# Performance work log

Hardware: AMD Instinct MI355X
Metric: run time of the kernel (lower is better)

Reference implementation:

```python
import jax, jax.numpy as jnp
import numpy as np

D_OUT = 32


def mlp(x, Ws, bs):
    # Ws: (L+1, d, d), bs: (L+1, d); relu after hidden layers, linear output
    h = x
    n = Ws.shape[0]
    for i in range(n - 1):
        h = jax.nn.relu(h @ Ws[i] + bs[i])
    return h @ Ws[n - 1] + bs[n - 1]


def causal_dot_product(Q, K, V, t1, t2):
    """out[:,:,i] = Q_i @ sum_{j: t2[j] <= t1[i]} K_j V_j^T.
    t2 is sorted (timestamps), so the cumulative outer-product state can be
    computed with a cumsum and gathered via searchsorted.
    Q: (1,1,T1,d); K,V: (1,1,T2,d); t1: (T1,); t2: (T2,).
    """
    outer = K[..., :, :, None] * V[..., :, None, :]      # (1,1,T2,d,d)
    S = jnp.cumsum(outer, axis=2)                        # prefix states
    idx = jnp.searchsorted(t2, t1, side='right') - 1     # (T1,)
    valid = idx >= 0
    Sg = S[:, :, jnp.maximum(idx, 0)]                    # (1,1,T1,d,d)
    out = jnp.einsum('bhid,bhide->bhie', Q, Sg)
    return jnp.where(valid[None, None, :, None], out, jnp.zeros((), out.dtype))


def _with_sorted_time(x, key):
    T = x.shape[2]
    t = jnp.sort(jax.random.uniform(key, (T,), dtype=jnp.float32)) * 100.0
    return x.at[0, 0, :, -1].set(t)


def setup_inputs() -> dict:
    key = jax.random.key(0)
    ks = jax.random.split(key, 16)
    d = 64
    Ts = [4096, 6144, 8192, 4096]
    mods = {}
    for i, T in enumerate(Ts):
        x = jax.random.normal(ks[i], (1, 1, T, d), dtype=jnp.float32)
        mods[f'm{i+1}'] = _with_sorted_time(x, ks[8 + i])
    scale = 1.0 / np.sqrt(d)
    WQ_w = jax.random.normal(ks[4], (3, d, d), dtype=jnp.float32) * scale
    WQ_b = jnp.zeros((3, d), dtype=jnp.float32)
    WK_w = jax.random.normal(ks[5], (4, 3, d, d), dtype=jnp.float32) * scale
    WK_b = jnp.zeros((4, 3, d), dtype=jnp.float32)
    return dict(m1=mods['m1'], m2=mods['m2'], m3=mods['m3'], m4=mods['m4'],
                WQ_w=WQ_w, WQ_b=WQ_b, WK_w=WK_w, WK_b=WK_b)


def reference(m1, m2, m3, m4, WQ_w, WQ_b, WK_w, WK_b):
    Q = mlp(m1, WQ_w, WQ_b)            # (1,1,T1,d)
    t1 = m1[0, 0, :, -1]               # (T1,)
    total = None
    for mi, X in enumerate([m1, m2, m3, m4]):
        K = mlp(X, WK_w[mi], WK_b[mi])
        V = X
        t2 = X[0, 0, :, -1]
        Z = causal_dot_product(Q, K, V, t1, t2)  # (1,1,T1,d)
        total = Z if total is None else total + Z
    # cat over dim=1 then sum(1) == sum of per-modality results, dim 1 dropped
    yhat = total.sum(axis=1)[..., :D_OUT]        # (1,T1,d_out)
    return yhat
```

## Files before the change

### kernel.cpp

```cpp
#include <hip/hip_runtime.h>


#define QB_OFF   0
#define KB_OFF   131072
#define SP_OFF   851968
#define TD_OFF   1581056
#define C_OFF    1603584

typedef __attribute__((ext_vector_type(8))) short short8;
typedef __attribute__((ext_vector_type(4))) float floatx4;

__device__ __forceinline__ unsigned short f2bf(float f) {
    union { float f; unsigned u; } v; v.f = f;
    unsigned r = v.u + 0x7fff + ((v.u >> 16) & 1);
    return (unsigned short)(r >> 16);
}

#define MFMA16(a,b,c) __builtin_amdgcn_mfma_f32_16x16x32_bf16((a),(b),(c),0,0,0)

__global__ __launch_bounds__(256) void k_fused(
    const float* __restrict__ x0, const float* __restrict__ x1,
    const float* __restrict__ x2, const float* __restrict__ x3,
    const float* __restrict__ wq_w, const float* __restrict__ wq_b,
    const float* __restrict__ wk_w, const float* __restrict__ wk_b,
    float* __restrict__ ws)
{
    __shared__ unsigned short H0[128*72];
    __shared__ unsigned short H1[128*72];
    __shared__ unsigned short Wt[64*72];
    __shared__ unsigned short KT[64*136];
    __shared__ unsigned short VT[32*136];

    const int tid = threadIdx.x;
    const int bid = blockIdx.x;

    int task, rb;
    if (bid < 32)       { task = 0; rb = bid; }
    else if (bid < 64)  { task = 1; rb = bid - 32; }
    else if (bid < 112) { task = 2; rb = bid - 64; }
    else if (bid < 176) { task = 3; rb = bid - 112; }
    else                { task = 4; rb = bid - 176; }

    const float* Xs[4] = {x0, x1, x2, x3};
    const int rowoff[4] = {0, 4096, 10240, 18432};
    const int spoff[4]  = {0, 65, 162, 291};

    const float* X; const float* W; const float* Bv;
    int mm = -1;
    if (task == 0) { X = x0; W = wq_w; Bv = wq_b; }
    else {
        mm = task - 1;
        X = Xs[mm]; W = wk_w + mm*3*64*64; Bv = wk_b + mm*3*64;
    }

    const int row0 = rb * 128;

    {
        const float4* X4 = (const float4*)(X + (size_t)row0*64);
        #pragma unroll
        for (int k = 0; k < 8; ++k) {
            int idx = k*256 + tid;
            float4 v = X4[idx];
            int rr = idx >> 4, c4 = (idx & 15) * 4;
            ushort4 h;
            h.x = f2bf(v.x); h.y = f2bf(v.y); h.z = f2bf(v.z); h.w = f2bf(v.w);
            *(ushort4*)&H0[rr*72 + c4] = h;
        }
    }
    if (task > 0 && tid < 128)
        ws[TD_OFF + rowoff[mm] + row0 + tid] = X[(size_t)(row0 + tid)*64 + 63];

    const int w    = tid >> 6;
    const int lane = tid & 63;
    const int lm   = lane & 15;
    const int q    = lane >> 4;

    #pragma unroll 1
    for (int l = 0; l < 3; ++l) {
        __syncthreads();
        {
            const float4* W4 = (const float4*)(W + l*4096);
            #pragma unroll
            for (int k = 0; k < 4; ++k) {
                int idx = k*256 + tid;
                float4 v = W4[idx];
                int d = idx >> 4, c4 = (idx & 15) * 4;
                Wt[(c4+0)*72 + d] = f2bf(v.x);
                Wt[(c4+1)*72 + d] = f2bf(v.y);
                Wt[(c4+2)*72 + d] = f2bf(v.z);
                Wt[(c4+3)*72 + d] = f2bf(v.w);
            }
        }
        __syncthreads();

        const unsigned short* Hin  = (l & 1) ? H1 : H0;
        unsigned short*       Hout = (l & 1) ? H0 : H1;
        float bias = Bv[l*64 + w*16 + lm];
        short8 b0 = *(const short8*)&Wt[(w*16+lm)*72 + q*8];
        short8 b1 = *(const short8*)&Wt[(w*16+lm)*72 + 32 + q*8];
        #pragma unroll
        for (int mt = 0; mt < 8; ++mt) {
            floatx4 acc = {bias, bias, bias, bias};
            short8 a0 = *(const short8*)&Hin[(mt*16+lm)*72 + q*8];
            short8 a1 = *(const short8*)&Hin[(mt*16+lm)*72 + 32 + q*8];
            acc = MFMA16(a0, b0, acc);
            acc = MFMA16(a1, b1, acc);
            int r0 = mt*16 + q*4;
            #pragma unroll
            for (int r = 0; r < 4; ++r) {
                float f = acc[r];
                if (l < 2) f = fmaxf(f, 0.0f);
                unsigned short hb = f2bf(f);
                Hout[(r0+r)*72 + w*16 + lm] = hb;
                if (l == 2 && task > 0)
                    KT[(w*16+lm)*136 + r0 + r] = hb;
            }
        }
    }
    __syncthreads();

    {
        unsigned short* dst = (task == 0)
            ? (unsigned short*)(ws + QB_OFF)
            : (unsigned short*)(ws + KB_OFF) + (size_t)rowoff[mm]*64;
        #pragma unroll
        for (int k = 0; k < 8; ++k) {
            int idx = k*256 + tid;
            int rr = idx >> 4, c4 = (idx & 15) * 4;
            *(ushort4*)&dst[(size_t)(row0 + rr)*64 + c4] = *(ushort4*)&H1[rr*72 + c4];
        }
    }
    if (task == 0) return;

    {
        #pragma unroll
        for (int k = 0; k < 4; ++k) {
            int idx = k*256 + tid;
            int j = idx >> 3, e4 = (idx & 7) * 4;
            float4 v = *(const float4*)&X[(size_t)(row0 + j)*64 + e4];
            VT[(e4+0)*136 + j] = f2bf(v.x);
            VT[(e4+1)*136 + j] = f2bf(v.y);
            VT[(e4+2)*136 + j] = f2bf(v.z);
            VT[(e4+3)*136 + j] = f2bf(v.w);
        }
    }
    float* spbase = ws + SP_OFF + (size_t)spoff[mm]*2048;
    if (rb == 0)
        for (int idx = tid; idx < 2048; idx += 256) spbase[idx] = 0.0f;
    __syncthreads();

    #pragma unroll 1
    for (int c = 0; c < 2; ++c) {
        float* slot = spbase + (size_t)(2*rb + c + 1) * 2048;
        #pragma unroll
        for (int nt = 0; nt < 2; ++nt) {
            floatx4 acc = {0.f, 0.f, 0.f, 0.f};
            #pragma unroll
            for (int ks = 0; ks < 2; ++ks) {
                short8 a = *(const short8*)&KT[(w*16+lm)*136 + c*64 + ks*32 + q*8];
                short8 b = *(const short8*)&VT[(nt*16+lm)*136 + c*64 + ks*32 + q*8];
                acc = MFMA16(a, b, acc);
            }
            #pragma unroll
            for (int r = 0; r < 4; ++r) {
                int d = w*16 + q*4 + r;
                int e = nt*16 + lm;
                slot[d*32 + e] = acc[r];
            }
        }
    }
}

__global__ __launch_bounds__(64) void k_prefix(float* __restrict__ ws)
{
    const int nslots[4] = {65, 97, 129, 65};
    const int spoff[4]  = {0, 65, 162, 291};
    const int Tm[4]     = {4096, 6144, 8192, 4096};
    const int rowoff[4] = {0, 4096, 10240, 18432};
    const int bid = blockIdx.x;

    if (bid < 128) {
        const int m = bid >> 5;
        const int entry = (bid & 31)*64 + threadIdx.x;
        float* p = ws + SP_OFF + (size_t)spoff[m]*2048 + entry;
        const int n = nslots[m];
        float s = 0.0f;
        #pragma unroll 8
        for (int k = 0; k < n; ++k) {
            float v = p[(size_t)k*2048];
            s += v;
            p[(size_t)k*2048] = s;
        }
        return;
    }
    const float* td = ws + TD_OFF;
    int* ctab = (int*)(ws + C_OFF);
    #pragma unroll 1
    for (int k = 0; k < 4; ++k) {
        int g = (bid - 128)*256 + k*64 + threadIdx.x;
        int m = g >> 7;
        int tile = (g >> 1) & 63;
        int bound = g & 1;
        float t = td[tile*64 + (bound ? 63 : 0)];
        const float* t2 = td + rowoff[m];
        int lo = 0, hi = Tm[m];
        while (lo < hi) {
            int mid = (lo + hi) >> 1;
            if (t2[mid] <= t) lo = mid + 1; else hi = mid;
        }
        ctab[g] = lo;
    }
}

__global__ __launch_bounds__(256) void k_query(
    const float* __restrict__ x0, const float* __restrict__ x1,
    const float* __restrict__ x2, const float* __restrict__ x3,
    float* __restrict__ ws, float* __restrict__ out)
{
    __shared__ unsigned short qs[64*72];
    __shared__ unsigned short kc[64*72];
    __shared__ unsigned short vt[32*72];
    __shared__ unsigned short st[32*72];
    __shared__ unsigned short ps[64*72];
    __shared__ float tq[64];
    __shared__ float tcs[64];

    const int tid  = threadIdx.x;
    const int m    = blockIdx.x & 3;
    const int tile = blockIdx.x >> 2;
    const int i0   = tile * 64;

    const float* Xs[4] = {x0, x1, x2, x3};
    const int rowoff[4] = {0, 4096, 10240, 18432};
    const int spoff[4]  = {0, 65, 162, 291};
    const float* X = Xs[m];

    const int* ctab = (const int*)(ws + C_OFF);
    const int c_lo = ctab[m*128 + tile*2 + 0];
    const int c_hi = ctab[m*128 + tile*2 + 1];
    const int B0   = c_lo >> 6;
    const int Bhi  = (c_hi + 63) >> 6;

    const unsigned short* Qg = (const unsigned short*)(ws + QB_OFF);
    const unsigned short* Kg = (const unsigned short*)(ws + KB_OFF) + (size_t)rowoff[m]*64;
    const float* td = ws + TD_OFF;
    const float* sp = ws + SP_OFF + (size_t)(spoff[m] + B0)*2048;

    {
        #pragma unroll
        for (int k = 0; k < 4; ++k) {
            int idx = k*256 + tid;
            int rr = idx >> 4, c4 = (idx & 15) * 4;
            *(ushort4*)&qs[rr*72 + c4] = *(const ushort4*)&Qg[(size_t)(i0 + rr)*64 + c4];
        }
        #pragma unroll
        for (int k = 0; k < 8; ++k) {
            int idx = k*256 + tid;
            int d = idx >> 5, e = idx & 31;
            st[e*72 + d] = f2bf(sp[idx]);
        }
        if (tid < 64) tq[tid] = td[i0 + tid];
    }
    __syncthreads();

    const int w    = tid >> 6;
    const int lane = tid & 63;
    const int lm   = lane & 15;
    const int q    = lane >> 4;

    float t1v[16];
    #pragma unroll
    for (int mt = 0; mt < 4; ++mt)
        #pragma unroll
        for (int r = 0; r < 4; ++r)
            t1v[mt*4 + r] = tq[mt*16 + q*4 + r];

    short8 qa[4][2];
    #pragma unroll
    for (int mt = 0; mt < 4; ++mt) {
        qa[mt][0] = *(const short8*)&qs[(mt*16+lm)*72 + q*8];
        qa[mt][1] = *(const short8*)&qs[(mt*16+lm)*72 + 32 + q*8];
    }

    floatx4 accO[2];
    #pragma unroll
    for (int nt = 0; nt < 2; ++nt) {
        floatx4 acc = {0.f, 0.f, 0.f, 0.f};
        #pragma unroll
        for (int ks = 0; ks < 2; ++ks) {
            short8 b = *(const short8*)&st[(nt*16+lm)*72 + ks*32 + q*8];
            acc = MFMA16(qa[w][ks], b, acc);
        }
        accO[nt] = acc;
    }

    #pragma unroll 1
    for (int B = B0; B < Bhi; ++B) {
        __syncthreads();
        #pragma unroll
        for (int k = 0; k < 4; ++k) {
            int idx = k*256 + tid;
            int j = idx >> 4, c4 = (idx & 15) * 4;
            *(ushort4*)&kc[j*72 + c4] = *(const ushort4*)&Kg[(size_t)(B*64 + j)*64 + c4];
        }
        #pragma unroll
        for (int k = 0; k < 2; ++k) {
            int idx = k*256 + tid;
            int j = idx >> 3, e4 = (idx & 7) * 4;
            float4 v = *(const float4*)&X[(size_t)(B*64 + j)*64 + e4];
            vt[(e4+0)*72 + j] = f2bf(v.x);
            vt[(e4+1)*72 + j] = f2bf(v.y);
            vt[(e4+2)*72 + j] = f2bf(v.z);
            vt[(e4+3)*72 + j] = f2bf(v.w);
        }
        if (tid < 64) tcs[tid] = td[rowoff[m] + B*64 + tid];
        __syncthreads();

        {
            short8 bk0 = *(const short8*)&kc[(w*16+lm)*72 + q*8];
            short8 bk1 = *(const short8*)&kc[(w*16+lm)*72 + 32 + q*8];
            float t2j = tcs[w*16 + lm];
            #pragma unroll
            for (int mt = 0; mt < 4; ++mt) {
                floatx4 f = {0.f, 0.f, 0.f, 0.f};
                f = MFMA16(qa[mt][0], bk0, f);
                f = MFMA16(qa[mt][1], bk1, f);
                #pragma unroll
                for (int r = 0; r < 4; ++r) {
                    float p = (t2j <= t1v[mt*4 + r]) ? f[r] : 0.0f;
                    ps[(mt*16 + q*4 + r)*72 + w*16 + lm] = f2bf(p);
                }
            }
        }
        __syncthreads();

        {
            short8 pa0 = *(const short8*)&ps[(w*16+lm)*72 + q*8];
            short8 pa1 = *(const short8*)&ps[(w*16+lm)*72 + 32 + q*8];
            #pragma unroll
            for (int nt = 0; nt < 2; ++nt) {
                short8 bv0 = *(const short8*)&vt[(nt*16+lm)*72 + q*8];
                short8 bv1 = *(const short8*)&vt[(nt*16+lm)*72 + 32 + q*8];
                accO[nt] = MFMA16(pa0, bv0, accO[nt]);
                accO[nt] = MFMA16(pa1, bv1, accO[nt]);
            }
        }
    }

    #pragma unroll
    for (int nt = 0; nt < 2; ++nt)
        #pragma unroll
        for (int r = 0; r < 4; ++r) {
            int i = w*16 + q*4 + r;
            int e = nt*16 + lm;
            atomicAdd(&out[(size_t)(i0 + i)*32 + e], accO[nt][r]);
        }
}

extern "C" void kernel_launch(void* const* d_in, const int* in_sizes, int n_in,
                              void* d_out, int out_size, void* d_ws, size_t ws_size,
                              hipStream_t stream) {
    const float* x0   = (const float*)d_in[0];
    const float* x1   = (const float*)d_in[1];
    const float* x2   = (const float*)d_in[2];
    const float* x3   = (const float*)d_in[3];
    const float* wq_w = (const float*)d_in[4];
    const float* wq_b = (const float*)d_in[5];
    const float* wk_w = (const float*)d_in[6];
    const float* wk_b = (const float*)d_in[7];
    float* ws  = (float*)d_ws;
    float* out = (float*)d_out;

    hipMemsetAsync(out, 0, (size_t)out_size * sizeof(float), stream);
    hipLaunchKernelGGL(k_fused,  dim3(208), dim3(256), 0, stream,
                       x0, x1, x2, x3, wq_w, wq_b, wk_w, wk_b, ws);
    hipLaunchKernelGGL(k_prefix, dim3(130), dim3(64),  0, stream, ws);
    hipLaunchKernelGGL(k_query,  dim3(256), dim3(256), 0, stream,
                       x0, x1, x2, x3, ws, out);
}
```

Before: 115.6 us.

## Fuse MLP, prefix and query kernels into one cooperative kernel with grid syncs

Replaces the memset plus three separate kernel launches with a single cooperative kernel that uses grid-wide syncs between the MLP/state phase, the prefix-sum/searchsorted phase, and the query phase. Spare blocks zero the output in place of the memset. MLP weights are now held in registers, loaded directly from global memory, rather than staged through a transposed shared-memory tile, and shared memory is unioned across phases. The goal is to remove launch and inter-kernel gaps. In exchange, the prefix phase runs on only 32 blocks with longer per-thread chains, and the kernel pays for cooperative launch and grid barriers.

```diff
diff --git a/kernel.cpp b/kernel.cpp
--- a/kernel.cpp
+++ b/kernel.cpp
@@ -1,4 +1,7 @@
 #include <hip/hip_runtime.h>
+#include <hip/hip_cooperative_groups.h>
+
+namespace cg = cooperative_groups;
 
 
 #define QB_OFF   0
@@ -18,170 +21,177 @@
 
 #define MFMA16(a,b,c) __builtin_amdgcn_mfma_f32_16x16x32_bf16((a),(b),(c),0,0,0)
 
-__global__ __launch_bounds__(256) void k_fused(
+struct P1 {
+    unsigned short H[128*72];
+    unsigned short KT[64*136];
+    unsigned short VT[32*136];
+};
+struct P3 {
+    unsigned short qs[64*72];
+    unsigned short kc[64*72];
+    unsigned short vt[32*72];
+    unsigned short st[32*72];
+    unsigned short ps[64*72];
+    float tq[64];
+    float tcs[64];
+};
+union __align__(16) SMem { P1 p1; P3 p3; };
+
+__global__ __launch_bounds__(256) void k_all(
     const float* __restrict__ x0, const float* __restrict__ x1,
     const float* __restrict__ x2, const float* __restrict__ x3,
     const float* __restrict__ wq_w, const float* __restrict__ wq_b,
     const float* __restrict__ wk_w, const float* __restrict__ wk_b,
-    float* __restrict__ ws)
+    float* __restrict__ ws, float* __restrict__ out)
 {
-    __shared__ unsigned short H0[128*72];
-    __shared__ unsigned short H1[128*72];
-    __shared__ unsigned short Wt[64*72];
-    __shared__ unsigned short KT[64*136];
-    __shared__ unsigned short VT[32*136];
+    __shared__ SMem sm;
+    cg::grid_group grid = cg::this_grid();
 
     const int tid = threadIdx.x;
     const int bid = blockIdx.x;
-
-    int task, rb;
-    if (bid < 32)       { task = 0; rb = bid; }
-    else if (bid < 64)  { task = 1; rb = bid - 32; }
-    else if (bid < 112) { task = 2; rb = bid - 64; }
-    else if (bid < 176) { task = 3; rb = bid - 112; }
-    else                { task = 4; rb = bid - 176; }
-
     const float* Xs[4] = {x0, x1, x2, x3};
     const int rowoff[4] = {0, 4096, 10240, 18432};
     const int spoff[4]  = {0, 65, 162, 291};
-
-    const float* X; const float* W; const float* Bv;
-    int mm = -1;
-    if (task == 0) { X = x0; W = wq_w; Bv = wq_b; }
-    else {
-        mm = task - 1;
-        X = Xs[mm]; W = wk_w + mm*3*64*64; Bv = wk_b + mm*3*64;
-    }
-
-    const int row0 = rb * 128;
-
-    {
-        const float4* X4 = (const float4*)(X + (size_t)row0*64);
-        #pragma unroll
-        for (int k = 0; k < 8; ++k) {
-            int idx = k*256 + tid;
-            float4 v = X4[idx];
-            int rr = idx >> 4, c4 = (idx & 15) * 4;
-            ushort4 h;
-            h.x = f2bf(v.x); h.y = f2bf(v.y); h.z = f2bf(v.z); h.w = f2bf(v.w);
-            *(ushort4*)&H0[rr*72 + c4] = h;
-        }
-    }
-    if (task > 0 && tid < 128)
-        ws[TD_OFF + rowoff[mm] + row0 + tid] = X[(size_t)(row0 + tid)*64 + 63];
 
     const int w    = tid >> 6;
     const int lane = tid & 63;
     const int lm   = lane & 15;
     const int q    = lane >> 4;
-
-    #pragma unroll 1
-    for (int l = 0; l < 3; ++l) {
+    const int col  = w*16 + lm;
+
+    if (bid >= 208) {
+        float4 z = make_float4(0.f, 0.f, 0.f, 0.f);
+        for (int i = (bid-208)*256 + tid; i < 32768; i += 12288)
+            ((float4*)out)[i] = z;
+    } else {
+        int task, rb;
+        if (bid < 32)       { task = 0; rb = bid; }
+        else if (bid < 64)  { task = 1; rb = bid - 32; }
+        else if (bid < 112) { task = 2; rb = bid - 64; }
+        else if (bid < 176) { task = 3; rb = bid - 112; }
+        else                { task = 4; rb = bid - 176; }
+
+        const float* X; const float* W; const float* Bv; int mm = -1;
+        if (task == 0) { X = x0; W = wq_w; Bv = wq_b; }
+        else {
+            mm = task - 1;
+            X = Xs[mm]; W = wk_w + mm*3*64*64; Bv = wk_b + mm*3*64;
+        }
+        const int row0 = rb * 128;
+
+        short8 wb[3][2]; float bias[3];
+        #pragma unroll
+        for (int l = 0; l < 3; ++l) {
+            bias[l] = Bv[l*64 + col];
+            #pragma unroll
+            for (int ks = 0; ks < 2; ++ks) {
+                short8 b;
+                #pragma unroll
+                for (int j = 0; j < 8; ++j)
+                    b[j] = (short)f2bf(W[l*4096 + (ks*32 + q*8 + j)*64 + col]);
+                wb[l][ks] = b;
+            }
+        }
+
+        {
+            const float4* X4 = (const float4*)(X + (size_t)row0*64);
+            #pragma unroll
+            for (int k = 0; k < 8; ++k) {
+                int idx = k*256 + tid;
+                float4 v = X4[idx];
+                int rr = idx >> 4, c4 = (idx & 15) * 4;
+                ushort4 h;
+                h.x = f2bf(v.x); h.y = f2bf(v.y); h.z = f2bf(v.z); h.w = f2bf(v.w);
+                *(ushort4*)&sm.p1.H[rr*72 + c4] = h;
+            }
+        }
+        if (task > 0 && tid < 128)
+            ws[TD_OFF + rowoff[mm] + row0 + tid] = X[(size_t)(row0 + tid)*64 + 63];
         __syncthreads();
+
+        #pragma unroll 1
+        for (int l = 0; l < 3; ++l) {
+            short8 a[8][2];
+            #pragma unroll
+            for (int mt = 0; mt < 8; ++mt) {
+                a[mt][0] = *(const short8*)&sm.p1.H[(mt*16+lm)*72 + q*8];
+                a[mt][1] = *(const short8*)&sm.p1.H[(mt*16+lm)*72 + 32 + q*8];
+            }
+            __syncthreads();
+            #pragma unroll
+            for (int mt = 0; mt < 8; ++mt) {
+                floatx4 acc = {bias[l], bias[l], bias[l], bias[l]};
+                acc = MFMA16(a[mt][0], wb[l][0], acc);
+                acc = MFMA16(a[mt][1], wb[l][1], acc);
+                int r0 = mt*16 + q*4;
+                #pragma unroll
+                for (int r = 0; r < 4; ++r) {
+                    float f = acc[r];
+                    if (l < 2) f = fmaxf(f, 0.0f);
+                    unsigned short hb = f2bf(f);
+                    sm.p1.H[(r0+r)*72 + col] = hb;
+                    if (l == 2 && task > 0) sm.p1.KT[col*136 + r0 + r] = hb;
+                }
+            }
+            __syncthreads();
+        }
+
         {
-            const float4* W4 = (const float4*)(W + l*4096);
+            unsigned short* dst = (task == 0)
+                ? (unsigned short*)(ws + QB_OFF)
+                : (unsigned short*)(ws + KB_OFF) + (size_t)rowoff[mm]*64;
+            #pragma unroll
+            for (int k = 0; k < 8; ++k) {
+                int idx = k*256 + tid;
+                int rr = idx >> 4, c4 = (idx & 15) * 4;
+                *(ushort4*)&dst[(size_t)(row0 + rr)*64 + c4] =
+                    *(ushort4*)&sm.p1.H[rr*72 + c4];
+            }
+        }
+
+        if (task > 0) {
             #pragma unroll
             for (int k = 0; k < 4; ++k) {
                 int idx = k*256 + tid;
-                float4 v = W4[idx];
-                int d = idx >> 4, c4 = (idx & 15) * 4;
-                Wt[(c4+0)*72 + d] = f2bf(v.x);
-                Wt[(c4+1)*72 + d] = f2bf(v.y);
-                Wt[(c4+2)*72 + d] = f2bf(v.z);
-                Wt[(c4+3)*72 + d] = f2bf(v.w);
-            }
-        }
-        __syncthreads();
-
-        const unsigned short* Hin  = (l & 1) ? H1 : H0;
-        unsigned short*       Hout = (l & 1) ? H0 : H1;
-        float bias = Bv[l*64 + w*16 + lm];
-        short8 b0 = *(const short8*)&Wt[(w*16+lm)*72 + q*8];
-        short8 b1 = *(const short8*)&Wt[(w*16+lm)*72 + 32 + q*8];
-        #pragma unroll
-        for (int mt = 0; mt < 8; ++mt) {
-            floatx4 acc = {bias, bias, bias, bias};
-            short8 a0 = *(const short8*)&Hin[(mt*16+lm)*72 + q*8];
-            short8 a1 = *(const short8*)&Hin[(mt*16+lm)*72 + 32 + q*8];
-            acc = MFMA16(a0, b0, acc);
-            acc = MFMA16(a1, b1, acc);
-            int r0 = mt*16 + q*4;
-            #pragma unroll
-            for (int r = 0; r < 4; ++r) {
-                float f = acc[r];
-                if (l < 2) f = fmaxf(f, 0.0f);
-                unsigned short hb = f2bf(f);
-                Hout[(r0+r)*72 + w*16 + lm] = hb;
-                if (l == 2 && task > 0)
-                    KT[(w*16+lm)*136 + r0 + r] = hb;
+                int j = idx >> 3, e4 = (idx & 7) * 4;
+                float4 v = *(const float4*)&X[(size_t)(row0 + j)*64 + e4];
+                sm.p1.VT[(e4+0)*136 + j] = f2bf(v.x);
+                sm.p1.VT[(e4+1)*136 + j] = f2bf(v.y);
+                sm.p1.VT[(e4+2)*136 + j] = f2bf(v.z);
+                sm.p1.VT[(e4+3)*136 + j] = f2bf(v.w);
+            }
+            float* spbase = ws + SP_OFF + (size_t)spoff[mm]*2048;
+            if (rb == 0)
+                for (int idx = tid; idx < 2048; idx += 256) spbase[idx] = 0.0f;
+            __syncthreads();
+
+            #pragma unroll 1
+            for (int cc = 0; cc < 2; ++cc) {
+                float* slot = spbase + (size_t)(2*rb + cc + 1) * 2048;
+                #pragma unroll
+                for (int nt = 0; nt < 2; ++nt) {
+                    floatx4 acc = {0.f, 0.f, 0.f, 0.f};
+                    #pragma unroll
+                    for (int ks = 0; ks < 2; ++ks) {
+                        short8 aa = *(const short8*)&sm.p1.KT[col*136 + cc*64 + ks*32 + q*8];
+                        short8 bb = *(const short8*)&sm.p1.VT[(nt*16+lm)*136 + cc*64 + ks*32 + q*8];
+                        acc = MFMA16(aa, bb, acc);
+                    }
+                    #pragma unroll
+                    for (int r = 0; r < 4; ++r)
+                        slot[(w*16 + q*4 + r)*32 + nt*16 + lm] = acc[r];
+                }
             }
         }
     }
-    __syncthreads();
-
-    {
-        unsigned short* dst = (task == 0)
-            ? (unsigned short*)(ws + QB_OFF)
-            : (unsigned short*)(ws + KB_OFF) + (size_t)rowoff[mm]*64;
-        #pragma unroll
-        for (int k = 0; k < 8; ++k) {
-            int idx = k*256 + tid;
-            int rr = idx >> 4, c4 = (idx & 15) * 4;
-            *(ushort4*)&dst[(size_t)(row0 + rr)*64 + c4] = *(ushort4*)&H1[rr*72 + c4];
-        }
-    }
-    if (task == 0) return;
-
-    {
-        #pragma unroll
-        for (int k = 0; k < 4; ++k) {
-            int idx = k*256 + tid;
-            int j = idx >> 3, e4 = (idx & 7) * 4;
-            float4 v = *(const float4*)&X[(size_t)(row0 + j)*64 + e4];
-            VT[(e4+0)*136 + j] = f2bf(v.x);
-            VT[(e4+1)*136 + j] = f2bf(v.y);
-            VT[(e4+2)*136 + j] = f2bf(v.z);
-            VT[(e4+3)*136 + j] = f2bf(v.w);
-        }
-    }
-    float* spbase = ws + SP_OFF + (size_t)spoff[mm]*2048;
-    if (rb == 0)
-        for (int idx = tid; idx < 2048; idx += 256) spbase[idx] = 0.0f;
-    __syncthreads();
-
-    #pragma unroll 1
-    for (int c = 0; c < 2; ++c) {
-        float* slot = spbase + (size_t)(2*rb + c + 1) * 2048;
-        #pragma unroll
-        for (int nt = 0; nt < 2; ++nt) {
-            floatx4 acc = {0.f, 0.f, 0.f, 0.f};
-            #pragma unroll
-            for (int ks = 0; ks < 2; ++ks) {
-                short8 a = *(const short8*)&KT[(w*16+lm)*136 + c*64 + ks*32 + q*8];
-                short8 b = *(const short8*)&VT[(nt*16+lm)*136 + c*64 + ks*32 + q*8];
-                acc = MFMA16(a, b, acc);
-            }
-            #pragma unroll
-            for (int r = 0; r < 4; ++r) {
-                int d = w*16 + q*4 + r;
-                int e = nt*16 + lm;
-                slot[d*32 + e] = acc[r];
-            }
-        }
-    }
-}
-
-__global__ __launch_bounds__(64) void k_prefix(float* __restrict__ ws)
-{
-    const int nslots[4] = {65, 97, 129, 65};
-    const int spoff[4]  = {0, 65, 162, 291};
-    const int Tm[4]     = {4096, 6144, 8192, 4096};
-    const int rowoff[4] = {0, 4096, 10240, 18432};
-    const int bid = blockIdx.x;
-
-    if (bid < 128) {
-        const int m = bid >> 5;
-        const int entry = (bid & 31)*64 + threadIdx.x;
+
+    __threadfence();
+    grid.sync();
+
+    if (bid < 32) {
+        const int nslots[4] = {65, 97, 129, 65};
+        int chain = bid*256 + tid;
+        int m = chain >> 11, entry = chain & 2047;
         float* p = ws + SP_OFF + (size_t)spoff[m]*2048 + entry;
         const int n = nslots[m];
         float s = 0.0f;
@@ -191,16 +201,12 @@
             s += v;
             p[(size_t)k*2048] = s;
         }
-        return;
-    }
-    const float* td = ws + TD_OFF;
-    int* ctab = (int*)(ws + C_OFF);
-    #pragma unroll 1
-    for (int k = 0; k < 4; ++k) {
-        int g = (bid - 128)*256 + k*64 + threadIdx.x;
-        int m = g >> 7;
-        int tile = (g >> 1) & 63;
-        int bound = g & 1;
+    } else if (bid < 34) {
+        const int Tm[4] = {4096, 6144, 8192, 4096};
+        const float* td = ws + TD_OFF;
+        int* ctab = (int*)(ws + C_OFF);
+        int g = (bid - 32)*256 + tid;
+        int m = g >> 7, tile = (g >> 1) & 63, bound = g & 1;
         float t = td[tile*64 + (bound ? 63 : 0)];
         const float* t2 = td + rowoff[m];
         int lo = 0, hi = Tm[m];
@@ -210,151 +216,132 @@
         }
         ctab[g] = lo;
     }
-}
-
-__global__ __launch_bounds__(256) void k_query(
-    const float* __restrict__ x0, const float* __restrict__ x1,
-    const float* __restrict__ x2, const float* __restrict__ x3,
-    float* __restrict__ ws, float* __restrict__ out)
-{
-    __shared__ unsigned short qs[64*72];
-    __shared__ unsigned short kc[64*72];
-    __shared__ unsigned short vt[32*72];
-    __shared__ unsigned short st[32*72];
-    __shared__ unsigned short ps[64*72];
-    __shared__ float tq[64];
-    __shared__ float tcs[64];
-
-    const int tid  = threadIdx.x;
-    const int m    = blockIdx.x & 3;
-    const int tile = blockIdx.x >> 2;
-    const int i0   = tile * 64;
-
-    const float* Xs[4] = {x0, x1, x2, x3};
-    const int rowoff[4] = {0, 4096, 10240, 18432};
-    const int spoff[4]  = {0, 65, 162, 291};
-    const float* X = Xs[m];
-
-    const int* ctab = (const int*)(ws + C_OFF);
-    const int c_lo = ctab[m*128 + tile*2 + 0];
-    const int c_hi = ctab[m*128 + tile*2 + 1];
-    const int B0   = c_lo >> 6;
-    const int Bhi  = (c_hi + 63) >> 6;
-
-    const unsigned short* Qg = (const unsigned short*)(ws + QB_OFF);
-    const unsigned short* Kg = (const unsigned short*)(ws + KB_OFF) + (size_t)rowoff[m]*64;
-    const float* td = ws + TD_OFF;
-    const float* sp = ws + SP_OFF + (size_t)(spoff[m] + B0)*2048;
+
+    __threadfence();
+    grid.sync();
 
     {
+        const int m    = bid & 3;
+        const int tile = bid >> 2;
+        const int i0   = tile * 64;
+        const float* X = Xs[m];
+
+        const int* ctab = (const int*)(ws + C_OFF);
+        const int c_lo = ctab[m*128 + tile*2 + 0];
+        const int c_hi = ctab[m*128 + tile*2 + 1];
+        const int B0   = c_lo >> 6;
+        const int Bhi  = (c_hi + 63) >> 6;
+
+        const unsigned short* Qg = (const unsigned short*)(ws + QB_OFF);
+        const unsigned short* Kg = (const unsigned short*)(ws + KB_OFF) + (size_t)rowoff[m]*64;
+        const float* td = ws + TD_OFF;
+        const float* sp = ws + SP_OFF + (size_t)(spoff[m] + B0)*2048;
+
         #pragma unroll
         for (int k = 0; k < 4; ++k) {
             int idx = k*256 + tid;
             int rr = idx >> 4, c4 = (idx & 15) * 4;
-            *(ushort4*)&qs[rr*72 + c4] = *(const ushort4*)&Qg[(size_t)(i0 + rr)*64 + c4];
+            *(ushort4*)&sm.p3.qs[rr*72 + c4] =
+                *(const ushort4*)&Qg[(size_t)(i0 + rr)*64 + c4];
         }
         #pragma unroll
         for (int k = 0; k < 8; ++k) {
             int idx = k*256 + tid;
             int d = idx >> 5, e = idx & 31;
-            st[e*72 + d] = f2bf(sp[idx]);
-        }
-        if (tid < 64) tq[tid] = td[i0 + tid];
+            sm.p3.st[e*72 + d] = f2bf(sp[idx]);
+        }
+        if (tid < 64) sm.p3.tq[tid] = td[i0 + tid];
+        __syncthreads();
+
+        float t1v[16];
+        #pragma unroll
+        for (int mt = 0; mt < 4; ++mt)
+            #pragma unroll
+            for (int r = 0; r < 4; ++r)
+                t1v[mt*4 + r] = sm.p3.tq[mt*16 + q*4 + r];
+
+        short8 qa[4][2];
+        #pragma unroll
+        for (int mt = 0; mt < 4; ++mt) {
+            qa[mt][0] = *(const short8*)&sm.p3.qs[(mt*16+lm)*72 + q*8];
+            qa[mt][1] = *(const short8*)&sm.p3.qs[(mt*16+lm)*72 + 32 + q*8];
+        }
+
+        floatx4 accO[2];
+        #pragma unroll
+        for (int nt = 0; nt < 2; ++nt) {
+            floatx4 acc = {0.f, 0.f, 0.f, 0.f};
+            #pragma unroll
+            for (int ks = 0; ks < 2; ++ks) {
+                short8 b = *(const short8*)&sm.p3.st[(nt*16+lm)*72 + ks*32 + q*8];
+                acc = MFMA16(qa[w][ks], b, acc);
+            }
+            accO[nt] = acc;
+        }
+
+        #pragma unroll 1
+        for (int B = B0; B < Bhi; ++B) {
+            __syncthreads();
+            #pragma unroll
+            for (int k = 0; k < 4; ++k) {
+                int idx = k*256 + tid;
+                int j = idx >> 4, c4 = (idx & 15) * 4;
+                *(ushort4*)&sm.p3.kc[j*72 + c4] =
+                    *(const ushort4*)&Kg[(size_t)(B*64 + j)*64 + c4];
+            }
+            #pragma unroll
+            for (int k = 0; k < 2; ++k) {
+                int idx = k*256 + tid;
+                int j = idx >> 3, e4 = (idx & 7) * 4;
+                float4 v = *(const float4*)&X[(size_t)(B*64 + j)*64 + e4];
+                sm.p3.vt[(e4+0)*72 + j] = f2bf(v.x);
+                sm.p3.vt[(e4+1)*72 + j] = f2bf(v.y);
+                sm.p3.vt[(e4+2)*72 + j] = f2bf(v.z);
+                sm.p3.vt[(e4+3)*72 + j] = f2bf(v.w);
+            }
+            if (tid < 64) sm.p3.tcs[tid] = td[rowoff[m] + B*64 + tid];
+            __syncthreads();
+
+            {
+                short8 bk0 = *(const short8*)&sm.p3.kc[(w*16+lm)*72 + q*8];
+                short8 bk1 = *(const short8*)&sm.p3.kc[(w*16+lm)*72 + 32 + q*8];
+                float t2j = sm.p3.tcs[w*16 + lm];
+                #pragma unroll
+                for (int mt = 0; mt < 4; ++mt) {
+                    floatx4 f = {0.f, 0.f, 0.f, 0.f};
+                    f = MFMA16(qa[mt][0], bk0, f);
+                    f = MFMA16(qa[mt][1], bk1, f);
+                    #pragma unroll
+                    for (int r = 0; r < 4; ++r) {
+                        float p = (t2j <= t1v[mt*4 + r]) ? f[r] : 0.0f;
+                        sm.p3.ps[(mt*16 + q*4 + r)*72 + w*16 + lm] = f2bf(p);
+                    }
+                }
+            }
+            __syncthreads();
+
+            {
+                short8 pa0 = *(const short8*)&sm.p3.ps[(w*16+lm)*72 + q*8];
+                short8 pa1 = *(const short8*)&sm.p3.ps[(w*16+lm)*72 + 32 + q*8];
+                #pragma unroll
+                for (int nt = 0; nt < 2; ++nt) {
+                    short8 bv0 = *(const short8*)&sm.p3.vt[(nt*16+lm)*72 + q*8];
+                    short8 bv1 = *(const short8*)&sm.p3.vt[(nt*16+lm)*72 + 32 + q*8];
+                    accO[nt] = MFMA16(pa0, bv0, accO[nt]);
+                    accO[nt] = MFMA16(pa1, bv1, accO[nt]);
+                }
+            }
+        }
+
+        #pragma unroll
+        for (int nt = 0; nt < 2; ++nt)
+            #pragma unroll
+            for (int r = 0; r < 4; ++r) {
+                int i = w*16 + q*4 + r;
+                int e = nt*16 + lm;
+                atomicAdd(&out[(size_t)(i0 + i)*32 + e], accO[nt][r]);
+            }
     }
-    __syncthreads();
-
-    const int w    = tid >> 6;
-    const int lane = tid & 63;
-    const int lm   = lane & 15;
-    const int q    = lane >> 4;
-
-    float t1v[16];
-    #pragma unroll
-    for (int mt = 0; mt < 4; ++mt)
-        #pragma unroll
-        for (int r = 0; r < 4; ++r)
-            t1v[mt*4 + r] = tq[mt*16 + q*4 + r];
-
-    short8 qa[4][2];
-    #pragma unroll
-    for (int mt = 0; mt < 4; ++mt) {
-        qa[mt][0] = *(const short8*)&qs[(mt*16+lm)*72 + q*8];
-        qa[mt][1] = *(const short8*)&qs[(mt*16+lm)*72 + 32 + q*8];
-    }
-
-    floatx4 accO[2];
-    #pragma unroll
-    for (int nt = 0; nt < 2; ++nt) {
-        floatx4 acc = {0.f, 0.f, 0.f, 0.f};
-        #pragma unroll
-        for (int ks = 0; ks < 2; ++ks) {
-            short8 b = *(const short8*)&st[(nt*16+lm)*72 + ks*32 + q*8];
-            acc = MFMA16(qa[w][ks], b, acc);
-        }
-        accO[nt] = acc;
-    }
-
-    #pragma unroll 1
-    for (int B = B0; B < Bhi; ++B) {
-        __syncthreads();
-        #pragma unroll
-        for (int k = 0; k < 4; ++k) {
-            int idx = k*256 + tid;
-            int j = idx >> 4, c4 = (idx & 15) * 4;
-            *(ushort4*)&kc[j*72 + c4] = *(const ushort4*)&Kg[(size_t)(B*64 + j)*64 + c4];
-        }
-        #pragma unroll
-        for (int k = 0; k < 2; ++k) {
-            int idx = k*256 + tid;
-            int j = idx >> 3, e4 = (idx & 7) * 4;
-            float4 v = *(const float4*)&X[(size_t)(B*64 + j)*64 + e4];
-            vt[(e4+0)*72 + j] = f2bf(v.x);
-            vt[(e4+1)*72 + j] = f2bf(v.y);
-            vt[(e4+2)*72 + j] = f2bf(v.z);
-            vt[(e4+3)*72 + j] = f2bf(v.w);
-        }
-        if (tid < 64) tcs[tid] = td[rowoff[m] + B*64 + tid];
-        __syncthreads();
-
-        {
-            short8 bk0 = *(const short8*)&kc[(w*16+lm)*72 + q*8];
-            short8 bk1 = *(const short8*)&kc[(w*16+lm)*72 + 32 + q*8];
-            float t2j = tcs[w*16 + lm];
-            #pragma unroll
-            for (int mt = 0; mt < 4; ++mt) {
-                floatx4 f = {0.f, 0.f, 0.f, 0.f};
-                f = MFMA16(qa[mt][0], bk0, f);
-                f = MFMA16(qa[mt][1], bk1, f);
-                #pragma unroll
-                for (int r = 0; r < 4; ++r) {
-                    float p = (t2j <= t1v[mt*4 + r]) ? f[r] : 0.0f;
-                    ps[(mt*16 + q*4 + r)*72 + w*16 + lm] = f2bf(p);
-                }
-            }
-        }
-        __syncthreads();
-
-        {
-            short8 pa0 = *(const short8*)&ps[(w*16+lm)*72 + q*8];
-            short8 pa1 = *(const short8*)&ps[(w*16+lm)*72 + 32 + q*8];
-            #pragma unroll
-            for (int nt = 0; nt < 2; ++nt) {
-                short8 bv0 = *(const short8*)&vt[(nt*16+lm)*72 + q*8];
-                short8 bv1 = *(const short8*)&vt[(nt*16+lm)*72 + 32 + q*8];
-                accO[nt] = MFMA16(pa0, bv0, accO[nt]);
-                accO[nt] = MFMA16(pa1, bv1, accO[nt]);
-            }
-        }
-    }
-
-    #pragma unroll
-    for (int nt = 0; nt < 2; ++nt)
-        #pragma unroll
-        for (int r = 0; r < 4; ++r) {
-            int i = w*16 + q*4 + r;
-            int e = nt*16 + lm;
-            atomicAdd(&out[(size_t)(i0 + i)*32 + e], accO[nt][r]);
-        }
 }
 
 extern "C" void kernel_launch(void* const* d_in, const int* in_sizes, int n_in,
@@ -371,10 +358,9 @@
     float* ws  = (float*)d_ws;
     float* out = (float*)d_out;
 
-    hipMemsetAsync(out, 0, (size_t)out_size * sizeof(float), stream);
-    hipLaunchKernelGGL(k_fused,  dim3(208), dim3(256), 0, stream,
-                       x0, x1, x2, x3, wq_w, wq_b, wk_w, wk_b, ws);
-    hipLaunchKernelGGL(k_prefix, dim3(130), dim3(64),  0, stream, ws);
-    hipLaunchKernelGGL(k_query,  dim3(256), dim3(256), 0, stream,
-                       x0, x1, x2, x3, ws, out);
+    void* args[] = {(void*)&x0, (void*)&x1, (void*)&x2, (void*)&x3,
+                    (void*)&wq_w, (void*)&wq_b, (void*)&wk_w, (void*)&wk_b,
+                    (void*)&ws, (void*)&out};
+    hipLaunchCooperativeKernel((const void*)k_all, dim3(256), dim3(256),
+                               args, 0, stream);
 }
```

Measured after the change: 252.1 us. 2.18x slower.

## Halve MLP row tiles, keep weights in registers, fold output zeroing into kernel

Applied to the files above, without the earlier changes.

The fused MLP/outer-product kernel now handles 64 rows per block instead of 128, doubling the grid to 416 blocks so more CUs are busy. Weights are loaded straight into per-thread bf16 registers for all three layers rather than being transposed through shared memory each layer, which removes two barriers per layer. The separate hipMemsetAsync of the output is dropped and the Q-task blocks zero it instead, saving a launch. Prefix slots now correspond to 64-row chunks, matching the old per-chunk layout, at the cost of repeated weight loads per block and strided global reads for the weights.

```diff
diff --git a/kernel.cpp b/kernel.cpp
--- a/kernel.cpp
+++ b/kernel.cpp
@@ -23,42 +23,65 @@
     const float* __restrict__ x2, const float* __restrict__ x3,
     const float* __restrict__ wq_w, const float* __restrict__ wq_b,
     const float* __restrict__ wk_w, const float* __restrict__ wk_b,
-    float* __restrict__ ws)
+    float* __restrict__ ws, float* __restrict__ out)
 {
-    __shared__ unsigned short H0[128*72];
-    __shared__ unsigned short H1[128*72];
-    __shared__ unsigned short Wt[64*72];
-    __shared__ unsigned short KT[64*136];
-    __shared__ unsigned short VT[32*136];
+    __shared__ unsigned short H0[64*72];
+    __shared__ unsigned short H1[64*72];
+    __shared__ unsigned short KT[64*72];
+    __shared__ unsigned short VT[32*72];
 
     const int tid = threadIdx.x;
     const int bid = blockIdx.x;
 
     int task, rb;
-    if (bid < 32)       { task = 0; rb = bid; }
-    else if (bid < 64)  { task = 1; rb = bid - 32; }
-    else if (bid < 112) { task = 2; rb = bid - 64; }
-    else if (bid < 176) { task = 3; rb = bid - 112; }
-    else                { task = 4; rb = bid - 176; }
+    if (bid < 64)       { task = 0; rb = bid; }
+    else if (bid < 128) { task = 1; rb = bid - 64; }
+    else if (bid < 224) { task = 2; rb = bid - 128; }
+    else if (bid < 352) { task = 3; rb = bid - 224; }
+    else                { task = 4; rb = bid - 352; }
 
     const float* Xs[4] = {x0, x1, x2, x3};
     const int rowoff[4] = {0, 4096, 10240, 18432};
     const int spoff[4]  = {0, 65, 162, 291};
 
-    const float* X; const float* W; const float* Bv;
-    int mm = -1;
+    const float* X; const float* W; const float* Bv; int mm = -1;
     if (task == 0) { X = x0; W = wq_w; Bv = wq_b; }
     else {
         mm = task - 1;
         X = Xs[mm]; W = wk_w + mm*3*64*64; Bv = wk_b + mm*3*64;
     }
 
-    const int row0 = rb * 128;
-
+    const int w    = tid >> 6;
+    const int lane = tid & 63;
+    const int lm   = lane & 15;
+    const int q    = lane >> 4;
+    const int col  = w*16 + lm;
+
+    if (task == 0) {
+        float4 z = make_float4(0.f, 0.f, 0.f, 0.f);
+        ((float4*)out)[bid*512 + tid]       = z;
+        ((float4*)out)[bid*512 + 256 + tid] = z;
+    }
+
+    short8 wb[3][2]; float bias[3];
+    #pragma unroll
+    for (int l = 0; l < 3; ++l) {
+        bias[l] = Bv[l*64 + col];
+        #pragma unroll
+        for (int ks = 0; ks < 2; ++ks) {
+            short8 b;
+            #pragma unroll
+            for (int j = 0; j < 8; ++j)
+                b[j] = (short)f2bf(W[l*4096 + (ks*32 + q*8 + j)*64 + col]);
+            wb[l][ks] = b;
+        }
+    }
+
+    const int row0 = rb * 64;
     {
         const float4* X4 = (const float4*)(X + (size_t)row0*64);
         #pragma unroll
-        for (int k = 0; k < 8; ++k) {
+        for (int k = 0; k < 4; ++k) {
             int idx = k*256 + tid;
             float4 v = X4[idx];
             int rr = idx >> 4, c4 = (idx & 15) * 4;
@@ -67,64 +90,40 @@
             *(ushort4*)&H0[rr*72 + c4] = h;
         }
     }
-    if (task > 0 && tid < 128)
+    if (task > 0 && tid < 64)
         ws[TD_OFF + rowoff[mm] + row0 + tid] = X[(size_t)(row0 + tid)*64 + 63];
-
-    const int w    = tid >> 6;
-    const int lane = tid & 63;
-    const int lm   = lane & 15;
-    const int q    = lane >> 4;
+    __syncthreads();
 
     #pragma unroll 1
     for (int l = 0; l < 3; ++l) {
-        __syncthreads();
-        {
-            const float4* W4 = (const float4*)(W + l*4096);
-            #pragma unroll
-            for (int k = 0; k < 4; ++k) {
-                int idx = k*256 + tid;
-                float4 v = W4[idx];
-                int d = idx >> 4, c4 = (idx & 15) * 4;
-                Wt[(c4+0)*72 + d] = f2bf(v.x);
-                Wt[(c4+1)*72 + d] = f2bf(v.y);
-                Wt[(c4+2)*72 + d] = f2bf(v.z);
-                Wt[(c4+3)*72 + d] = f2bf(v.w);
-            }
-        }
-        __syncthreads();
-
         const unsigned short* Hin  = (l & 1) ? H1 : H0;
         unsigned short*       Hout = (l & 1) ? H0 : H1;
-        float bias = Bv[l*64 + w*16 + lm];
-        short8 b0 = *(const short8*)&Wt[(w*16+lm)*72 + q*8];
-        short8 b1 = *(const short8*)&Wt[(w*16+lm)*72 + 32 + q*8];
-        #pragma unroll
-        for (int mt = 0; mt < 8; ++mt) {
-            floatx4 acc = {bias, bias, bias, bias};
+        #pragma unroll
+        for (int mt = 0; mt < 4; ++mt) {
             short8 a0 = *(const short8*)&Hin[(mt*16+lm)*72 + q*8];
             short8 a1 = *(const short8*)&Hin[(mt*16+lm)*72 + 32 + q*8];
-            acc = MFMA16(a0, b0, acc);
-            acc = MFMA16(a1, b1, acc);
+            floatx4 acc = {bias[l], bias[l], bias[l], bias[l]};
+            acc = MFMA16(a0, wb[l][0], acc);
+            acc = MFMA16(a1, wb[l][1], acc);
             int r0 = mt*16 + q*4;
             #pragma unroll
             for (int r = 0; r < 4; ++r) {
                 float f = acc[r];
                 if (l < 2) f = fmaxf(f, 0.0f);
                 unsigned short hb = f2bf(f);
-                Hout[(r0+r)*72 + w*16 + lm] = hb;
-                if (l == 2 && task > 0)
-                    KT[(w*16+lm)*136 + r0 + r] = hb;
+                Hout[(r0+r)*72 + col] = hb;
+                if (l == 2 && task > 0) KT[col*72 + r0 + r] = hb;
             }
         }
-    }
-    __syncthreads();
+        __syncthreads();
+    }
 
     {
         unsigned short* dst = (task == 0)
             ? (unsigned short*)(ws + QB_OFF)
             : (unsigned short*)(ws + KB_OFF) + (size_t)rowoff[mm]*64;
         #pragma unroll
-        for (int k = 0; k < 8; ++k) {
+        for (int k = 0; k < 4; ++k) {
             int idx = k*256 + tid;
             int rr = idx >> 4, c4 = (idx & 15) * 4;
             *(ushort4*)&dst[(size_t)(row0 + rr)*64 + c4] = *(ushort4*)&H1[rr*72 + c4];
@@ -134,14 +133,14 @@
 
     {
         #pragma unroll
-        for (int k = 0; k < 4; ++k) {
+        for (int k = 0; k < 2; ++k) {
             int idx = k*256 + tid;
             int j = idx >> 3, e4 = (idx & 7) * 4;
             float4 v = *(const float4*)&X[(size_t)(row0 + j)*64 + e4];
-            VT[(e4+0)*136 + j] = f2bf(v.x);
-            VT[(e4+1)*136 + j] = f2bf(v.y);
-            VT[(e4+2)*136 + j] = f2bf(v.z);
-            VT[(e4+3)*136 + j] = f2bf(v.w);
+            VT[(e4+0)*72 + j] = f2bf(v.x);
+            VT[(e4+1)*72 + j] = f2bf(v.y);
+            VT[(e4+2)*72 + j] = f2bf(v.z);
+            VT[(e4+3)*72 + j] = f2bf(v.w);
         }
     }
     float* spbase = ws + SP_OFF + (size_t)spoff[mm]*2048;
@@ -149,24 +148,20 @@
         for (int idx = tid; idx < 2048; idx += 256) spbase[idx] = 0.0f;
     __syncthreads();
 
-    #pragma unroll 1
-    for (int c = 0; c < 2; ++c) {
-        float* slot = spbase + (size_t)(2*rb + c + 1) * 2048;
+    {
+        float* slot = spbase + (size_t)(rb + 1) * 2048;
         #pragma unroll
         for (int nt = 0; nt < 2; ++nt) {
             floatx4 acc = {0.f, 0.f, 0.f, 0.f};
             #pragma unroll
             for (int ks = 0; ks < 2; ++ks) {
-                short8 a = *(const short8*)&KT[(w*16+lm)*136 + c*64 + ks*32 + q*8];
-                short8 b = *(const short8*)&VT[(nt*16+lm)*136 + c*64 + ks*32 + q*8];
-                acc = MFMA16(a, b, acc);
+                short8 aa = *(const short8*)&KT[col*72 + ks*32 + q*8];
+                short8 bb = *(const short8*)&VT[(nt*16+lm)*72 + ks*32 + q*8];
+                acc = MFMA16(aa, bb, acc);
             }
             #pragma unroll
-            for (int r = 0; r < 4; ++r) {
-                int d = w*16 + q*4 + r;
-                int e = nt*16 + lm;
-                slot[d*32 + e] = acc[r];
-            }
+            for (int r = 0; r < 4; ++r)
+                slot[(w*16 + q*4 + r)*32 + nt*16 + lm] = acc[r];
         }
     }
 }
@@ -246,21 +241,19 @@
     const float* td = ws + TD_OFF;
     const float* sp = ws + SP_OFF + (size_t)(spoff[m] + B0)*2048;
 
-    {
-        #pragma unroll
-        for (int k = 0; k < 4; ++k) {
-            int idx = k*256 + tid;
-            int rr = idx >> 4, c4 = (idx & 15) * 4;
-            *(ushort4*)&qs[rr*72 + c4] = *(const ushort4*)&Qg[(size_t)(i0 + rr)*64 + c4];
-        }
-        #pragma unroll
-        for (int k = 0; k < 8; ++k) {
-            int idx = k*256 + tid;
-            int d = idx >> 5, e = idx & 31;
-            st[e*72 + d] = f2bf(sp[idx]);
-        }
-        if (tid < 64) tq[tid] = td[i0 + tid];
-    }
+    #pragma unroll
+    for (int k = 0; k < 4; ++k) {
+        int idx = k*256 + tid;
+        int rr = idx >> 4, c4 = (idx & 15) * 4;
+        *(ushort4*)&qs[rr*72 + c4] = *(const ushort4*)&Qg[(size_t)(i0 + rr)*64 + c4];
+    }
+    #pragma unroll
+    for (int k = 0; k < 8; ++k) {
+        int idx = k*256 + tid;
+        int d = idx >> 5, e = idx & 31;
+        st[e*72 + d] = f2bf(sp[idx]);
+    }
+    if (tid < 64) tq[tid] = td[i0 + tid];
     __syncthreads();
 
     const int w    = tid >> 6;
@@ -371,9 +364,8 @@
     float* ws  = (float*)d_ws;
     float* out = (float*)d_out;
 
-    hipMemsetAsync(out, 0, (size_t)out_size * sizeof(float), stream);
-    hipLaunchKernelGGL(k_fused,  dim3(208), dim3(256), 0, stream,
-                       x0, x1, x2, x3, wq_w, wq_b, wk_w, wk_b, ws);
+    hipLaunchKernelGGL(k_fused,  dim3(416), dim3(256), 0, stream,
+                       x0, x1, x2, x3, wq_w, wq_b, wk_w, wk_b, ws, out);
     hipLaunchKernelGGL(k_prefix, dim3(130), dim3(64),  0, stream, ws);
     hipLaunchKernelGGL(k_query,  dim3(256), dim3(256), 0, stream,
                        x0, x1, x2, x3, ws, out);
```

Result: slower. 140.7 us (+21.7%).
